# Kernel tuning notes

Hardware: AMD Instinct MI355X
Metric: run time of the kernel (lower is better)

## Reference

```python
import jax, jax.numpy as jnp
import numpy as np

IN_FEATURES = 4096
OUT_FEATURES = 4096


def setup_inputs() -> dict:
    key = jax.random.key(0)
    k_x, k_w, k_ws, k_b = jax.random.split(key, 4)
    x = jax.random.normal(k_x, (4, 2048, IN_FEATURES), dtype=jnp.float16)
    # int8 weight in [-127, 127]
    weight = jax.random.randint(k_w, (OUT_FEATURES, IN_FEATURES), -127, 128, dtype=jnp.int32).astype(jnp.int8)
    # realistic small per-output-channel dequant scales (as produced by from_float)
    weight_scales = (jax.random.uniform(k_ws, (OUT_FEATURES,), dtype=jnp.float32) * 0.02 + 0.001).astype(jnp.float16)
    bias = (jax.random.normal(k_b, (1, OUT_FEATURES), dtype=jnp.float32) * 0.01).astype(jnp.float16)
    return {"x": x, "weight": weight, "weight_scales": weight_scales, "bias": bias}


def reference(x, weight, weight_scales, bias):
    x_shape = x.shape
    xf = x.reshape(-1, x_shape[-1]).astype(jnp.float32)  # [T, in]
    # dynamic per-token min-max quantization: scale = max|x| / 127
    x_scale = jnp.max(jnp.abs(xf), axis=-1, keepdims=True) / 127.0  # [T, 1]
    q_x = jnp.clip(jnp.round(xf / x_scale), -128, 127).astype(jnp.int8)  # [T, in]
    # int8 GEMM accumulated in int32: q_y = q_x @ weight.T
    q_y = jnp.matmul(q_x.astype(jnp.int32), weight.T.astype(jnp.int32))  # [T, out]
    # dequant: per-channel weight scale * per-token activation scale
    y = q_y.astype(jnp.float32) * weight_scales.astype(jnp.float32)[None, :] * x_scale
    y = y.astype(jnp.float16).reshape(*x_shape[:-1], -1)
    y = y + bias  # fp16 bias add, broadcasts [1, out]
    return y
```

## Files before the change

kernel.cpp:

```cpp
#include <hip/hip_runtime.h>
#include <hip/hip_bf16.h>
#include <stdint.h>

typedef int v4i __attribute__((ext_vector_type(4)));
typedef float v4f __attribute__((ext_vector_type(4)));

#define T_TOKENS 8192
#define KDIM 4096
#define NDIM 4096

#define BM 128
#define BN 128
#define BK 64

__global__ __launch_bounds__(256) void conv_w(const int* __restrict__ w32,
                                              int8_t* __restrict__ w8) {
    int idx = blockIdx.x * 256 + threadIdx.x;
    const v4i* src = (const v4i*)w32 + (size_t)idx * 4;
    v4i p;
#pragma unroll
    for (int q = 0; q < 4; ++q) {
        v4i s = src[q];
        p[q] = (s[0] & 255) | ((s[1] & 255) << 8) | ((s[2] & 255) << 16)
             | ((s[3] & 255) << 24);
    }
    ((v4i*)w8)[idx] = p;
}

__global__ __launch_bounds__(256) void quant_x(const float* __restrict__ x,
                                               int8_t* __restrict__ qx,
                                               float* __restrict__ xs) {
    int t = blockIdx.x;
    int tid = threadIdx.x;
    const v4f* xrow = (const v4f*)(x + (size_t)t * KDIM);

    v4f vals[4];
    float m = 0.f;
#pragma unroll
    for (int q = 0; q < 4; ++q) {
        v4f v = xrow[q * 256 + tid];
        vals[q] = v;
        m = fmaxf(m, fmaxf(fmaxf(fabsf(v[0]), fabsf(v[1])),
                           fmaxf(fabsf(v[2]), fabsf(v[3]))));
    }
#pragma unroll
    for (int off = 32; off > 0; off >>= 1)
        m = fmaxf(m, __shfl_xor(m, off));

    __shared__ float wmax[4];
    __shared__ float sh_scale;
    int wave = tid >> 6;
    if ((tid & 63) == 0) wmax[wave] = m;
    __syncthreads();
    if (tid == 0) {
        float mm = fmaxf(fmaxf(wmax[0], wmax[1]), fmaxf(wmax[2], wmax[3]));
        float sc = mm / 127.0f;
        sh_scale = sc;
        xs[t] = sc;
    }
    __syncthreads();
    float sc = sh_scale;

    unsigned int* qrow = (unsigned int*)(qx + (size_t)t * KDIM);
#pragma unroll
    for (int q = 0; q < 4; ++q) {
        unsigned int packed = 0;
#pragma unroll
        for (int j = 0; j < 4; ++j) {
            float fq = rintf(vals[q][j] / sc);
            fq = fminf(fmaxf(fq, -128.f), 127.f);
            int b = (int)fq;
            packed |= ((unsigned int)(unsigned char)(b & 0xff)) << (8 * j);
        }
        qrow[q * 256 + tid] = packed;
    }
}

__global__ __launch_bounds__(256) void gemm_i8(
        const int8_t* __restrict__ A, const int8_t* __restrict__ B,
        const float* __restrict__ xs, const float* __restrict__ wscale,
        const float* __restrict__ bias, float* __restrict__ out) {
    __shared__ char As[BM * BK];
    __shared__ char Bs[BN * BK];

    int tid = threadIdx.x;
    int lane = tid & 63;
    int wave = tid >> 6;
    int wr = wave >> 1, wc = wave & 1;
    int bm = blockIdx.x, bn = blockIdx.y;
    int lrow = lane & 15, kg = lane >> 4;

    const int8_t* Abase = A + (size_t)bm * BM * KDIM;
    const int8_t* Bbase = B + (size_t)bn * BN * KDIM;

    v4i acc[4][4] = {};

    for (int kt = 0; kt < KDIM / BK; ++kt) {
        int k0 = kt * BK;
#pragma unroll
        for (int it = 0; it < 2; ++it) {
            int idx = it * 256 + tid;
            int row = idx >> 2;
            int slot = idx & 3;
            int gcol = (slot ^ ((row >> 1) & 3)) << 4;
            const int8_t* ga = Abase + (size_t)row * KDIM + k0 + gcol;
            const int8_t* gb = Bbase + (size_t)row * KDIM + k0 + gcol;
            char* la = As + (size_t)(it * 256 + wave * 64) * 16;
            char* lb = Bs + (size_t)(it * 256 + wave * 64) * 16;
            __builtin_amdgcn_global_load_lds(
                (const __attribute__((address_space(1))) void*)ga,
                (__attribute__((address_space(3))) void*)la, 16, 0, 0);
            __builtin_amdgcn_global_load_lds(
                (const __attribute__((address_space(1))) void*)gb,
                (__attribute__((address_space(3))) void*)lb, 16, 0, 0);
        }
        __syncthreads();

        v4i af[4], bfr[4];
#pragma unroll
        for (int mm = 0; mm < 4; ++mm) {
            int r = wr * 64 + mm * 16 + lrow;
            int addr = r * BK + ((kg ^ ((r >> 1) & 3)) << 4);
            af[mm] = *(const v4i*)(As + addr);
        }
#pragma unroll
        for (int nn = 0; nn < 4; ++nn) {
            int r = wc * 64 + nn * 16 + lrow;
            int addr = r * BK + ((kg ^ ((r >> 1) & 3)) << 4);
            bfr[nn] = *(const v4i*)(Bs + addr);
        }
#pragma unroll
        for (int mm = 0; mm < 4; ++mm)
#pragma unroll
            for (int nn = 0; nn < 4; ++nn)
                acc[mm][nn] = __builtin_amdgcn_mfma_i32_16x16x64_i8(
                    af[mm], bfr[nn], acc[mm][nn], 0, 0, 0);
        __syncthreads();
    }

    int rowg0 = bm * BM + wr * 64;
    int colg0 = bn * BN + wc * 64;
    float xsv[4][4];
#pragma unroll
    for (int mm = 0; mm < 4; ++mm)
#pragma unroll
        for (int j = 0; j < 4; ++j)
            xsv[mm][j] = xs[rowg0 + mm * 16 + kg * 4 + j];

#pragma unroll
    for (int nn = 0; nn < 4; ++nn) {
        int col = colg0 + nn * 16 + lrow;
        float wsc = wscale[col];
        float bs = bias[col];
#pragma unroll
        for (int mm = 0; mm < 4; ++mm) {
#pragma unroll
            for (int j = 0; j < 4; ++j) {
                int row = rowg0 + mm * 16 + kg * 4 + j;
                float y = (float)acc[mm][nn][j] * wsc * xsv[mm][j] + bs;
                out[(size_t)row * NDIM + col] = y;
            }
        }
    }
}

extern "C" void kernel_launch(void* const* d_in, const int* in_sizes, int n_in,
                              void* d_out, int out_size, void* d_ws, size_t ws_size,
                              hipStream_t stream) {
    const float* x    = (const float*)d_in[0];
    const int*   w32  = (const int*)d_in[1];
    const float* wsc  = (const float*)d_in[2];
    const float* bias = (const float*)d_in[3];
    float* out = (float*)d_out;

    int8_t* qx = (int8_t*)d_ws;
    int8_t* w8 = (int8_t*)d_ws + (size_t)T_TOKENS * KDIM;
    float*  xs = (float*)((int8_t*)d_ws + (size_t)T_TOKENS * KDIM + (size_t)NDIM * KDIM);

    hipLaunchKernelGGL(conv_w, dim3(NDIM * KDIM / 16 / 256), dim3(256), 0, stream, w32, w8);
    hipLaunchKernelGGL(quant_x, dim3(T_TOKENS), dim3(256), 0, stream, x, qx, xs);
    hipLaunchKernelGGL(gemm_i8, dim3(T_TOKENS / BM, NDIM / BN), dim3(256), 0, stream,
                       qx, w8, xs, wsc, bias, out);
}
```

Before: 460.0 us.

## Double-buffer int8 GEMM with 256x256 tiles, 8 waves, and swizzled block order

Rewrites the int8 GEMM kernel to use 256x256 output tiles with 512 threads and a 128-byte K step. Global-to-LDS loads for the next K tile go into a second 64KB buffer while MFMAs run on the current one, with partial vmcnt waits and raw barriers in place of full syncthreads. Adds an XCD-aware remapping of the flattened block index and raises wave priority around the MFMA burst. This gives more data reuse per byte loaded and hides memory latency, at the cost of 128KB of LDS per block and a higher register count.

```diff
diff --git a/kernel.cpp b/kernel.cpp
--- a/kernel.cpp
+++ b/kernel.cpp
@@ -9,9 +9,9 @@
 #define KDIM 4096
 #define NDIM 4096
 
-#define BM 128
-#define BN 128
-#define BK 64
+#define BM 256
+#define BN 256
+#define BKB 128
 
 __global__ __launch_bounds__(256) void conv_w(const int* __restrict__ w32,
                                               int8_t* __restrict__ w8) {
@@ -76,92 +76,117 @@
     }
 }
 
-__global__ __launch_bounds__(256) void gemm_i8(
+__global__ __launch_bounds__(512, 2) void gemm_i8(
         const int8_t* __restrict__ A, const int8_t* __restrict__ B,
         const float* __restrict__ xs, const float* __restrict__ wscale,
         const float* __restrict__ bias, float* __restrict__ out) {
-    __shared__ char As[BM * BK];
-    __shared__ char Bs[BN * BK];
-
-    int tid = threadIdx.x;
-    int lane = tid & 63;
-    int wave = tid >> 6;
-    int wr = wave >> 1, wc = wave & 1;
-    int bm = blockIdx.x, bn = blockIdx.y;
-    int lrow = lane & 15, kg = lane >> 4;
-
-    const int8_t* Abase = A + (size_t)bm * BM * KDIM;
-    const int8_t* Bbase = B + (size_t)bn * BN * KDIM;
-
-    v4i acc[4][4] = {};
-
-    for (int kt = 0; kt < KDIM / BK; ++kt) {
-        int k0 = kt * BK;
-#pragma unroll
-        for (int it = 0; it < 2; ++it) {
-            int idx = it * 256 + tid;
-            int row = idx >> 2;
-            int slot = idx & 3;
-            int gcol = (slot ^ ((row >> 1) & 3)) << 4;
-            const int8_t* ga = Abase + (size_t)row * KDIM + k0 + gcol;
-            const int8_t* gb = Bbase + (size_t)row * KDIM + k0 + gcol;
-            char* la = As + (size_t)(it * 256 + wave * 64) * 16;
-            char* lb = Bs + (size_t)(it * 256 + wave * 64) * 16;
-            __builtin_amdgcn_global_load_lds(
-                (const __attribute__((address_space(1))) void*)ga,
-                (__attribute__((address_space(3))) void*)la, 16, 0, 0);
-            __builtin_amdgcn_global_load_lds(
-                (const __attribute__((address_space(1))) void*)gb,
-                (__attribute__((address_space(3))) void*)lb, 16, 0, 0);
+    __shared__ char lds[131072];
+
+    const int tid  = threadIdx.x;
+    const int lane = tid & 63;
+    const int w    = tid >> 6;
+    const int wr   = w >> 2;
+    const int wc   = w & 3;
+    const int lrow = lane & 15;
+    const int kg   = lane >> 4;
+    const int swz  = (kg ^ ((lrow >> 1) & 3)) << 4;
+
+    int flat = blockIdx.x;
+    int f2 = (flat & 7) * 64 + (flat >> 3);
+    int bm = f2 >> 4, bn = f2 & 15;
+
+    const int8_t* Ab = A + (size_t)bm * BM * KDIM;
+    const int8_t* Bb = B + (size_t)bn * BN * KDIM;
+
+    const int srow = (w << 5) + (lane >> 2);
+    const int sg16 = (((lane & 3) ^ ((lane >> 3) & 3)) << 4);
+    const size_t goff = (size_t)srow * KDIM + sg16;
+
+#define STAGE(gp, kbyte, lbase)                                                  \
+    do {                                                                         \
+        const int8_t* g0 = (gp) + goff + (kbyte);                                \
+        char* l0 = (lbase) + (w << 11);                                          \
+        __builtin_amdgcn_global_load_lds(                                        \
+            (const __attribute__((address_space(1))) void*)g0,                   \
+            (__attribute__((address_space(3))) void*)l0, 16, 0, 0);              \
+        __builtin_amdgcn_global_load_lds(                                        \
+            (const __attribute__((address_space(1))) void*)(g0 + (size_t)16 * KDIM), \
+            (__attribute__((address_space(3))) void*)(l0 + 1024), 16, 0, 0);     \
+    } while (0)
+
+    v4i acc[8][4] = {};
+
+    STAGE(Ab, 0,  lds + 0);
+    STAGE(Bb, 0,  lds + 32768);
+    STAGE(Ab, 64, lds + 16384);
+    STAGE(Bb, 64, lds + 49152);
+    asm volatile("s_waitcnt vmcnt(0)" ::: "memory");
+    __builtin_amdgcn_s_barrier();
+    asm volatile("" ::: "memory");
+
+    const int abase = wr * 128 + lrow;
+    const int bbase = wc * 64 + lrow;
+
+    for (int t = 0; t < KDIM / BKB; ++t) {
+        char* cur = lds + ((t & 1) << 16);
+        char* nxt = lds + (((t + 1) & 1) << 16);
+        int   nk  = ((t + 1) & 31) * BKB;
+
+#pragma unroll
+        for (int ks = 0; ks < 2; ++ks) {
+            STAGE(Ab, nk + ks * 64, nxt + ks * 16384);
+            STAGE(Bb, nk + ks * 64, nxt + 32768 + ks * 16384);
+
+            const char* ap = cur + ks * 16384;
+            const char* bp = cur + 32768 + ks * 16384;
+            v4i af[8], bf[4];
+#pragma unroll
+            for (int m = 0; m < 8; ++m)
+                af[m] = *(const v4i*)(ap + (abase + m * 16) * 64 + swz);
+#pragma unroll
+            for (int n = 0; n < 4; ++n)
+                bf[n] = *(const v4i*)(bp + (bbase + n * 16) * 64 + swz);
+
+            __builtin_amdgcn_s_setprio(1);
+#pragma unroll
+            for (int m = 0; m < 8; ++m)
+#pragma unroll
+                for (int n = 0; n < 4; ++n)
+                    acc[m][n] = __builtin_amdgcn_mfma_i32_16x16x64_i8(
+                        af[m], bf[n], acc[m][n], 0, 0, 0);
+            __builtin_amdgcn_s_setprio(0);
+
+            asm volatile("s_waitcnt vmcnt(4)" ::: "memory");
+            __builtin_amdgcn_s_barrier();
+            asm volatile("" ::: "memory");
         }
-        __syncthreads();
-
-        v4i af[4], bfr[4];
-#pragma unroll
-        for (int mm = 0; mm < 4; ++mm) {
-            int r = wr * 64 + mm * 16 + lrow;
-            int addr = r * BK + ((kg ^ ((r >> 1) & 3)) << 4);
-            af[mm] = *(const v4i*)(As + addr);
-        }
-#pragma unroll
-        for (int nn = 0; nn < 4; ++nn) {
-            int r = wc * 64 + nn * 16 + lrow;
-            int addr = r * BK + ((kg ^ ((r >> 1) & 3)) << 4);
-            bfr[nn] = *(const v4i*)(Bs + addr);
-        }
-#pragma unroll
-        for (int mm = 0; mm < 4; ++mm)
-#pragma unroll
-            for (int nn = 0; nn < 4; ++nn)
-                acc[mm][nn] = __builtin_amdgcn_mfma_i32_16x16x64_i8(
-                    af[mm], bfr[nn], acc[mm][nn], 0, 0, 0);
-        __syncthreads();
-    }
-
-    int rowg0 = bm * BM + wr * 64;
+    }
+
+    int rowg0 = bm * BM + wr * 128;
     int colg0 = bn * BN + wc * 64;
-    float xsv[4][4];
-#pragma unroll
-    for (int mm = 0; mm < 4; ++mm)
+    float xsv[8][4];
+#pragma unroll
+    for (int m = 0; m < 8; ++m)
 #pragma unroll
         for (int j = 0; j < 4; ++j)
-            xsv[mm][j] = xs[rowg0 + mm * 16 + kg * 4 + j];
-
-#pragma unroll
-    for (int nn = 0; nn < 4; ++nn) {
-        int col = colg0 + nn * 16 + lrow;
+            xsv[m][j] = xs[rowg0 + m * 16 + kg * 4 + j];
+
+#pragma unroll
+    for (int n = 0; n < 4; ++n) {
+        int col = colg0 + n * 16 + lrow;
         float wsc = wscale[col];
-        float bs = bias[col];
-#pragma unroll
-        for (int mm = 0; mm < 4; ++mm) {
+        float bs  = bias[col];
+#pragma unroll
+        for (int m = 0; m < 8; ++m) {
 #pragma unroll
             for (int j = 0; j < 4; ++j) {
-                int row = rowg0 + mm * 16 + kg * 4 + j;
-                float y = (float)acc[mm][nn][j] * wsc * xsv[mm][j] + bs;
+                int row = rowg0 + m * 16 + kg * 4 + j;
+                float y = (float)acc[m][n][j] * wsc * xsv[m][j] + bs;
                 out[(size_t)row * NDIM + col] = y;
             }
         }
     }
+#undef STAGE
 }
 
 extern "C" void kernel_launch(void* const* d_in, const int* in_sizes, int n_in,
@@ -179,6 +204,6 @@
 
     hipLaunchKernelGGL(conv_w, dim3(NDIM * KDIM / 16 / 256), dim3(256), 0, stream, w32, w8);
     hipLaunchKernelGGL(quant_x, dim3(T_TOKENS), dim3(256), 0, stream, x, qx, xs);
-    hipLaunchKernelGGL(gemm_i8, dim3(T_TOKENS / BM, NDIM / BN), dim3(256), 0, stream,
+    hipLaunchKernelGGL(gemm_i8, dim3((T_TOKENS / BM) * (NDIM / BN)), dim3(512), 0, stream,
                        qx, w8, xs, wsc, bias, out);
 }
```

New measurement: 393.1 us. -14.6%, faster.
